# Optimization experiments

Measured on AMD Instinct MI355X. Metric: run time of the kernel, lower is better.

The kernel has to match this reference:

```python
import jax, jax.numpy as jnp
import numpy as np

N = 50000      # nodes
IN = 256       # in_feat
H = 4          # num_heads
DH = 64        # out_feat // num_heads
R = 6          # number of relations
E = 300000     # edges per relation
NEG_SLOPE = 0.2  # DGL GATConv leaky_relu slope


def setup_inputs() -> dict:
    key = jax.random.key(0)
    ks = jax.random.split(key, 7)
    x = jax.random.normal(ks[0], (N, IN), dtype=jnp.float32)
    W = jax.random.normal(ks[1], (R, IN, H * DH), dtype=jnp.float32) * (1.0 / np.sqrt(IN))
    attn_l = jax.random.normal(ks[2], (R, H, DH), dtype=jnp.float32) * 0.1
    attn_r = jax.random.normal(ks[3], (R, H, DH), dtype=jnp.float32) * 0.1
    bias = jax.random.normal(ks[4], (R, H * DH), dtype=jnp.float32) * 0.01
    src = jax.random.randint(ks[5], (R, E), 0, N, dtype=jnp.int32).astype(jnp.int64)
    dst = jax.random.randint(ks[6], (R, E), 0, N, dtype=jnp.int32).astype(jnp.int64)
    return {"x": x, "W": W, "attn_l": attn_l, "attn_r": attn_r, "bias": bias,
            "src": src, "dst": dst}


def reference(x, W, attn_l, attn_r, bias, src, dst):
    n = x.shape[0]
    r_total, h, dh = attn_l.shape
    out = jnp.zeros((n, h, dh), dtype=x.dtype)
    # small fixed loop over structurally-distinct relations (HeteroGraphConv)
    for r in range(r_total):
        feat = (x @ W[r]).reshape(n, h, dh)            # [N,H,Dh] shared src/dst proj
        el = jnp.sum(feat * attn_l[r], axis=-1)        # [N,H]
        er = jnp.sum(feat * attn_r[r], axis=-1)        # [N,H]
        s, d = src[r], dst[r]
        e = jax.nn.leaky_relu(el[s] + er[d], NEG_SLOPE)  # [E,H]
        # segmented softmax over incoming edges of each dst node
        m = jax.ops.segment_max(e, d, num_segments=n)    # [N,H]
        m = jnp.where(jnp.isfinite(m), m, 0.0)
        a = jnp.exp(e - m[d])                            # [E,H]
        z = jax.ops.segment_sum(a, d, num_segments=n)    # [N,H]
        alpha = a / jnp.maximum(z[d], 1e-9)              # [E,H]
        msg = alpha[:, :, None] * feat[s]                # [E,H,Dh]
        agg = jax.ops.segment_sum(msg, d, num_segments=n)  # [N,H,Dh]
        # GATConv: bias + activation(relu) per relation, HeteroGraphConv sums
        out = out + jax.nn.relu(agg + bias[r].reshape(h, dh))
    hcat = out.reshape(n, h * dh)                        # merge='cat' view
    return jax.nn.relu(hcat)                             # layer-level activation
```

## Files before the change

### kernel.cpp

```cpp
#include <hip/hip_runtime.h>

#define NN 50000
#define MP 50048
#define NH 4
#define NR 6
#define NE 300000
#define HD 256
#define SLOTS 32
#define CHUNKS 64
#define CHSZ ((NE + CHUNKS - 1) / CHUNKS)

typedef __attribute__((ext_vector_type(4))) float f32x4;
typedef __attribute__((ext_vector_type(8))) short bf16x8;

__device__ __forceinline__ short f2bf(float f) {
  unsigned u = __float_as_uint(f);
  unsigned r = (u + 0x7FFFu + ((u >> 16) & 1u)) >> 16;
  return (short)r;
}
__device__ __forceinline__ float bf2f_lo(unsigned d) {
  return __uint_as_float(d << 16);
}
__device__ __forceinline__ float bf2f_hi(unsigned d) {
  return __uint_as_float(d & 0xffff0000u);
}

#define GLOAD_LDS16(g, l)                                                     \
  __builtin_amdgcn_global_load_lds(                                           \
      (const __attribute__((address_space(1))) void*)(g),                     \
      (__attribute__((address_space(3))) void*)(l), 16, 0, 0)

__global__ __launch_bounds__(256) void cast_x_kernel(
    const float* __restrict__ x, short* __restrict__ xb, int n4) {
  const int i = blockIdx.x * 256 + threadIdx.x;
  if (i >= n4) return;
  const float4 v = ((const float4*)x)[i];
  short4 o;
  o.x = f2bf(v.x); o.y = f2bf(v.y); o.z = f2bf(v.z); o.w = f2bf(v.w);
  ((short4*)xb)[i] = o;
}

__global__ __launch_bounds__(256) void cast_wt_kernel(
    const float* __restrict__ W, short* __restrict__ wt) {
  const int o = blockIdx.x * 256 + threadIdx.x;
  if (o >= NR * 256 * 256) return;
  const int r = o >> 16;
  const int nrow = (o >> 8) & 255;
  const int k = o & 255;
  wt[o] = f2bf(W[r * 65536 + k * 256 + nrow]);
}

__global__ __launch_bounds__(256) void gemm_kernel(
    const short* __restrict__ xb,
    const short* __restrict__ wt_all,
    const float* __restrict__ attn_l,
    const float* __restrict__ attn_r,
    short* __restrict__ featb_all,
    float* __restrict__ el_all, float* __restrict__ er_all) {
  __shared__ short As[128 * 32];
  __shared__ short Bs[128 * 32];
  const int t = threadIdx.x;
  const int lane = t & 63;
  const int w = t >> 6;
  const int wm = w & 1, wn = w >> 1;
  const int row0 = blockIdx.x * 128;
  const int n0 = blockIdx.y * 128;
  const int r = blockIdx.z;
  const short* wt = wt_all + (size_t)r * 65536;
  short* featb = featb_all + (size_t)r * MP * 256;

  f32x4 acc[4][4];
#pragma unroll
  for (int mi = 0; mi < 4; ++mi)
#pragma unroll
    for (int ni = 0; ni < 4; ++ni) {
      f32x4 z = {0.f, 0.f, 0.f, 0.f};
      acc[mi][ni] = z;
    }

  const int c0 = t, c1 = 256 + t;
  int ar0 = row0 + (c0 >> 2); if (ar0 >= NN) ar0 = NN - 1;
  int ar1 = row0 + (c1 >> 2); if (ar1 >= NN) ar1 = NN - 1;
  const short* ag0 = xb + (size_t)ar0 * 256 + (c0 & 3) * 8;
  const short* ag1 = xb + (size_t)ar1 * 256 + (c1 & 3) * 8;
  const short* bg0 = wt + (size_t)(n0 + (c0 >> 2)) * 256 + (c0 & 3) * 8;
  const short* bg1 = wt + (size_t)(n0 + (c1 >> 2)) * 256 + (c1 & 3) * 8;
  short* la0 = As + c0 * 8;
  short* la1 = As + c1 * 8;
  short* lb0 = Bs + c0 * 8;
  short* lb1 = Bs + c1 * 8;

  const int ra = lane & 15;
  const int qa = (lane >> 4) * 8;

  for (int k0 = 0; k0 < 256; k0 += 32) {
    GLOAD_LDS16(ag0 + k0, la0);
    GLOAD_LDS16(ag1 + k0, la1);
    GLOAD_LDS16(bg0 + k0, lb0);
    GLOAD_LDS16(bg1 + k0, lb1);
    __syncthreads();
    bf16x8 af[4], bfr[4];
#pragma unroll
    for (int mi = 0; mi < 4; ++mi)
      af[mi] = *(const bf16x8*)&As[(wm * 64 + mi * 16 + ra) * 32 + qa];
#pragma unroll
    for (int ni = 0; ni < 4; ++ni)
      bfr[ni] = *(const bf16x8*)&Bs[(wn * 64 + ni * 16 + ra) * 32 + qa];
#pragma unroll
    for (int mi = 0; mi < 4; ++mi)
#pragma unroll
      for (int ni = 0; ni < 4; ++ni)
        acc[mi][ni] = __builtin_amdgcn_mfma_f32_16x16x32_bf16(
            af[mi], bfr[ni], acc[mi][ni], 0, 0, 0);
    __syncthreads();
  }

  const int h = (n0 >> 6) + wn;
  float alv[4], arv[4];
#pragma unroll
  for (int ni = 0; ni < 4; ++ni) {
    alv[ni] = attn_l[r * HD + h * 64 + ni * 16 + ra];
    arv[ni] = attn_r[r * HD + h * 64 + ni * 16 + ra];
  }
#pragma unroll
  for (int mi = 0; mi < 4; ++mi) {
#pragma unroll
    for (int j = 0; j < 4; ++j) {
      const int row = row0 + wm * 64 + mi * 16 + (lane >> 4) * 4 + j;
      float elp = 0.f, erp = 0.f;
#pragma unroll
      for (int ni = 0; ni < 4; ++ni) {
        const float v = acc[mi][ni][j];
        featb[(size_t)row * 256 + n0 + wn * 64 + ni * 16 + ra] = f2bf(v);
        elp = fmaf(v, alv[ni], elp);
        erp = fmaf(v, arv[ni], erp);
      }
#pragma unroll
      for (int m = 1; m < 16; m <<= 1) {
        elp += __shfl_xor(elp, m, 64);
        erp += __shfl_xor(erp, m, 64);
      }
      if (ra == 0 && row < NN) {
        el_all[((size_t)r * NN + row) * NH + h] = elp;
        er_all[((size_t)r * NN + row) * NH + h] = erp;
      }
    }
  }
}

__global__ __launch_bounds__(256) void pack_kernel(
    const int* __restrict__ src, const int* __restrict__ dst,
    unsigned* __restrict__ pe) {
  const int i = blockIdx.x * 256 + threadIdx.x;
  if (i < NR * NE)
    pe[i] = ((unsigned)dst[i] << 16) | (unsigned)src[i];
}

__global__ __launch_bounds__(256) void build_kernel(
    const unsigned* __restrict__ pe, int* __restrict__ deg,
    unsigned short* __restrict__ slots) {
  const int grp = blockIdx.x & 7;
  const int chunk = blockIdx.x >> 3;
  const int lo = chunk * CHSZ;
  const int hi = (lo + CHSZ < NE) ? lo + CHSZ : NE;
  const unsigned dlo = grp * (NN / 8);
  for (int r = 0; r < NR; ++r) {
    for (int i = lo + threadIdx.x; i < hi; i += 256) {
      const unsigned p = pe[(size_t)r * NE + i];
      const unsigned d = p >> 16;
      if (d - dlo < (unsigned)(NN / 8)) {
        const int g = r * NN + (int)d;
        const int sl = atomicAdd(&deg[g], 1);
        if (sl < SLOTS)
          slots[(size_t)g * SLOTS + sl] = (unsigned short)(p & 0xffffu);
      }
    }
  }
}

__global__ __launch_bounds__(256) void agg_kernel(
    const short* __restrict__ featb_all, const float* __restrict__ el_all,
    const float* __restrict__ er_all, const int* __restrict__ deg,
    const unsigned short* __restrict__ slots, const float* __restrict__ bias,
    float* __restrict__ out) {
  const int wid = (blockIdx.x * 256 + threadIdx.x) >> 6;
  const int lane = threadIdx.x & 63;
  if (wid >= NN) return;
  const int half = lane >> 5;
  const int cl = lane & 31;
  const int h = cl >> 3;
  const int c0 = cl * 8;

  float oacc[8];
#pragma unroll
  for (int k = 0; k < 8; ++k) oacc[k] = 0.f;

  for (int r = 0; r < NR; ++r) {
    const int g = r * NN + wid;
    int dg = deg[g];
    dg = dg > SLOTS ? SLOTS : dg;
    const unsigned short* slp = slots + (size_t)g * SLOTS;
    const int sv = (lane < SLOTS) ? (int)slp[lane] : 0;
    const float er_nh = er_all[(size_t)g * NH + h];
    const float* elr = el_all + (size_t)r * NN * NH;
    const short* fb = featb_all + (size_t)r * MP * 256;

    float z = 0.f;
    float acc[8];
#pragma unroll
    for (int k = 0; k < 8; ++k) acc[k] = 0.f;

    const int iters = (dg + 1) >> 1;
    for (int j = 0; j < iters; ++j) {
      const int j2 = 2 * j + half;
      const bool valid = j2 < dg;
      int s = __shfl(sv, j2, 64);
      s = valid ? s : 0;
      float e = elr[s * NH + h] + er_nh;
      e = fmaxf(e, 0.2f * e);
      const float p = valid ? __expf(e) : 0.f;
      const uint4 raw = *(const uint4*)(fb + (size_t)s * 256 + c0);
      z += p;
      acc[0] = fmaf(p, bf2f_lo(raw.x), acc[0]);
      acc[1] = fmaf(p, bf2f_hi(raw.x), acc[1]);
      acc[2] = fmaf(p, bf2f_lo(raw.y), acc[2]);
      acc[3] = fmaf(p, bf2f_hi(raw.y), acc[3]);
      acc[4] = fmaf(p, bf2f_lo(raw.z), acc[4]);
      acc[5] = fmaf(p, bf2f_hi(raw.z), acc[5]);
      acc[6] = fmaf(p, bf2f_lo(raw.w), acc[6]);
      acc[7] = fmaf(p, bf2f_hi(raw.w), acc[7]);
    }
    z += __shfl_xor(z, 32, 64);
#pragma unroll
    for (int k = 0; k < 8; ++k) acc[k] += __shfl_xor(acc[k], 32, 64);
    const float inv = 1.f / fmaxf(z, 1e-9f);
    const float4 b0 = *(const float4*)(bias + r * HD + c0);
    const float4 b1 = *(const float4*)(bias + r * HD + c0 + 4);
    oacc[0] += fmaxf(fmaf(acc[0], inv, b0.x), 0.f);
    oacc[1] += fmaxf(fmaf(acc[1], inv, b0.y), 0.f);
    oacc[2] += fmaxf(fmaf(acc[2], inv, b0.z), 0.f);
    oacc[3] += fmaxf(fmaf(acc[3], inv, b0.w), 0.f);
    oacc[4] += fmaxf(fmaf(acc[4], inv, b1.x), 0.f);
    oacc[5] += fmaxf(fmaf(acc[5], inv, b1.y), 0.f);
    oacc[6] += fmaxf(fmaf(acc[6], inv, b1.z), 0.f);
    oacc[7] += fmaxf(fmaf(acc[7], inv, b1.w), 0.f);
  }
  if (half == 0) {
    float4 s0 = {oacc[0], oacc[1], oacc[2], oacc[3]};
    float4 s1 = {oacc[4], oacc[5], oacc[6], oacc[7]};
    *(float4*)(out + (size_t)wid * 256 + c0) = s0;
    *(float4*)(out + (size_t)wid * 256 + c0 + 4) = s1;
  }
}

extern "C" void kernel_launch(void* const* d_in, const int* in_sizes, int n_in,
                              void* d_out, int out_size, void* d_ws,
                              size_t ws_size, hipStream_t stream) {
  const float* x      = (const float*)d_in[0];
  const float* W      = (const float*)d_in[1];
  const float* attn_l = (const float*)d_in[2];
  const float* attn_r = (const float*)d_in[3];
  const float* bias   = (const float*)d_in[4];
  const int*   src    = (const int*)d_in[5];
  const int*   dst    = (const int*)d_in[6];
  float* out = (float*)d_out;

  char* p = (char*)d_ws;
  auto alloc = [&](size_t bytes) {
    char* r = p;
    p += (bytes + 255) & ~(size_t)255;
    return r;
  };
  short* xb    = (short*)alloc((size_t)NN * HD * 2);
  short* wt    = (short*)alloc((size_t)NR * 256 * 256 * 2);
  short* featb = (short*)alloc((size_t)NR * MP * 256 * 2);
  float* el    = (float*)alloc((size_t)NR * NN * NH * 4);
  float* er    = (float*)alloc((size_t)NR * NN * NH * 4);
  int*   deg   = (int*)alloc((size_t)NR * NN * 4);
  unsigned short* slots =
      (unsigned short*)alloc((size_t)NR * NN * SLOTS * 2);
  unsigned* pe = (unsigned*)alloc((size_t)NR * NE * 4);

  hipMemsetAsync(deg, 0, (size_t)NR * NN * 4, stream);

  cast_x_kernel<<<(NN * HD / 4 + 255) / 256, 256, 0, stream>>>(x, xb,
                                                               NN * HD / 4);
  cast_wt_kernel<<<(NR * 256 * 256 + 255) / 256, 256, 0, stream>>>(W, wt);
  pack_kernel<<<(NR * NE + 255) / 256, 256, 0, stream>>>(src, dst, pe);
  build_kernel<<<CHUNKS * 8, 256, 0, stream>>>(pe, deg, slots);
  gemm_kernel<<<dim3(MP / 128, 2, NR), 256, 0, stream>>>(xb, wt, attn_l,
                                                         attn_r, featb, el,
                                                         er);
  agg_kernel<<<(NN * 64) / 256, 256, 0, stream>>>(featb, el, er, deg, slots,
                                                  bias, out);
}
```

Measured before the change: 476.5 us.

## Remap aggregation wave to 4 columns per lane with scalarized slot indices

Each 64-lane wave now covers all 256 feature columns, 4 per lane, and processes one neighbor per step across the whole wave. The old scheme split the wave into two halves handling alternate edges and then combined them with cross-lane shuffles. Slot indices are loaded as wide vectors and moved into scalar registers with readfirstlane, replacing the per-edge shuffle. The edge loop is unrolled by 4 so several gathers are in flight at once. This removes the shuffle reduction and the half-idle iteration on odd degrees, at the cost of narrower 8-byte loads per lane, more scalar registers, and each wave walking the full edge list serially.

```diff
diff --git a/kernel.cpp b/kernel.cpp
--- a/kernel.cpp
+++ b/kernel.cpp
@@ -186,71 +186,79 @@
   const int wid = (blockIdx.x * 256 + threadIdx.x) >> 6;
   const int lane = threadIdx.x & 63;
   if (wid >= NN) return;
-  const int half = lane >> 5;
-  const int cl = lane & 31;
-  const int h = cl >> 3;
-  const int c0 = cl * 8;
-
-  float oacc[8];
-#pragma unroll
-  for (int k = 0; k < 8; ++k) oacc[k] = 0.f;
+  const int h = lane >> 4;
+  const int c0 = lane * 4;
+
+  float oacc[4] = {0.f, 0.f, 0.f, 0.f};
+  const int wid_u = __builtin_amdgcn_readfirstlane(wid);
 
   for (int r = 0; r < NR; ++r) {
-    const int g = r * NN + wid;
-    int dg = deg[g];
+    const int g = r * NN + wid_u;
+    int dg = __builtin_amdgcn_readfirstlane(deg[g]);
     dg = dg > SLOTS ? SLOTS : dg;
-    const unsigned short* slp = slots + (size_t)g * SLOTS;
-    const int sv = (lane < SLOTS) ? (int)slp[lane] : 0;
+    const uint4* sp = (const uint4*)(slots + (size_t)g * SLOTS);
+    const uint4 q0 = sp[0], q1 = sp[1], q2 = sp[2], q3 = sp[3];
+    unsigned sdv[16];
+    sdv[0]  = __builtin_amdgcn_readfirstlane(q0.x);
+    sdv[1]  = __builtin_amdgcn_readfirstlane(q0.y);
+    sdv[2]  = __builtin_amdgcn_readfirstlane(q0.z);
+    sdv[3]  = __builtin_amdgcn_readfirstlane(q0.w);
+    sdv[4]  = __builtin_amdgcn_readfirstlane(q1.x);
+    sdv[5]  = __builtin_amdgcn_readfirstlane(q1.y);
+    sdv[6]  = __builtin_amdgcn_readfirstlane(q1.z);
+    sdv[7]  = __builtin_amdgcn_readfirstlane(q1.w);
+    sdv[8]  = __builtin_amdgcn_readfirstlane(q2.x);
+    sdv[9]  = __builtin_amdgcn_readfirstlane(q2.y);
+    sdv[10] = __builtin_amdgcn_readfirstlane(q2.z);
+    sdv[11] = __builtin_amdgcn_readfirstlane(q2.w);
+    sdv[12] = __builtin_amdgcn_readfirstlane(q3.x);
+    sdv[13] = __builtin_amdgcn_readfirstlane(q3.y);
+    sdv[14] = __builtin_amdgcn_readfirstlane(q3.z);
+    sdv[15] = __builtin_amdgcn_readfirstlane(q3.w);
+
     const float er_nh = er_all[(size_t)g * NH + h];
     const float* elr = el_all + (size_t)r * NN * NH;
     const short* fb = featb_all + (size_t)r * MP * 256;
 
     float z = 0.f;
-    float acc[8];
-#pragma unroll
-    for (int k = 0; k < 8; ++k) acc[k] = 0.f;
-
-    const int iters = (dg + 1) >> 1;
-    for (int j = 0; j < iters; ++j) {
-      const int j2 = 2 * j + half;
-      const bool valid = j2 < dg;
-      int s = __shfl(sv, j2, 64);
-      s = valid ? s : 0;
-      float e = elr[s * NH + h] + er_nh;
-      e = fmaxf(e, 0.2f * e);
-      const float p = valid ? __expf(e) : 0.f;
-      const uint4 raw = *(const uint4*)(fb + (size_t)s * 256 + c0);
-      z += p;
-      acc[0] = fmaf(p, bf2f_lo(raw.x), acc[0]);
-      acc[1] = fmaf(p, bf2f_hi(raw.x), acc[1]);
-      acc[2] = fmaf(p, bf2f_lo(raw.y), acc[2]);
-      acc[3] = fmaf(p, bf2f_hi(raw.y), acc[3]);
-      acc[4] = fmaf(p, bf2f_lo(raw.z), acc[4]);
-      acc[5] = fmaf(p, bf2f_hi(raw.z), acc[5]);
-      acc[6] = fmaf(p, bf2f_lo(raw.w), acc[6]);
-      acc[7] = fmaf(p, bf2f_hi(raw.w), acc[7]);
+    float acc[4] = {0.f, 0.f, 0.f, 0.f};
+
+#pragma unroll
+    for (int j0 = 0; j0 < SLOTS; j0 += 4) {
+      if (j0 >= dg) break;
+      float pv[4];
+      uint2 rw[4];
+#pragma unroll
+      for (int k = 0; k < 4; ++k) {
+        const int e = j0 + k;
+        int s = (int)((e & 1) ? (sdv[e >> 1] >> 16) : (sdv[e >> 1] & 0xffffu));
+        const bool v = e < dg;
+        s = v ? s : 0;
+        rw[k] = *(const uint2*)(fb + (size_t)s * 256 + c0);
+        float ev = elr[s * NH + h] + er_nh;
+        ev = fmaxf(ev, 0.2f * ev);
+        pv[k] = v ? __expf(ev) : 0.f;
+      }
+#pragma unroll
+      for (int k = 0; k < 4; ++k) {
+        z += pv[k];
+        acc[0] = fmaf(pv[k], bf2f_lo(rw[k].x), acc[0]);
+        acc[1] = fmaf(pv[k], bf2f_hi(rw[k].x), acc[1]);
+        acc[2] = fmaf(pv[k], bf2f_lo(rw[k].y), acc[2]);
+        acc[3] = fmaf(pv[k], bf2f_hi(rw[k].y), acc[3]);
+      }
     }
-    z += __shfl_xor(z, 32, 64);
-#pragma unroll
-    for (int k = 0; k < 8; ++k) acc[k] += __shfl_xor(acc[k], 32, 64);
+
     const float inv = 1.f / fmaxf(z, 1e-9f);
-    const float4 b0 = *(const float4*)(bias + r * HD + c0);
-    const float4 b1 = *(const float4*)(bias + r * HD + c0 + 4);
-    oacc[0] += fmaxf(fmaf(acc[0], inv, b0.x), 0.f);
-    oacc[1] += fmaxf(fmaf(acc[1], inv, b0.y), 0.f);
-    oacc[2] += fmaxf(fmaf(acc[2], inv, b0.z), 0.f);
-    oacc[3] += fmaxf(fmaf(acc[3], inv, b0.w), 0.f);
-    oacc[4] += fmaxf(fmaf(acc[4], inv, b1.x), 0.f);
-    oacc[5] += fmaxf(fmaf(acc[5], inv, b1.y), 0.f);
-    oacc[6] += fmaxf(fmaf(acc[6], inv, b1.z), 0.f);
-    oacc[7] += fmaxf(fmaf(acc[7], inv, b1.w), 0.f);
-  }
-  if (half == 0) {
-    float4 s0 = {oacc[0], oacc[1], oacc[2], oacc[3]};
-    float4 s1 = {oacc[4], oacc[5], oacc[6], oacc[7]};
-    *(float4*)(out + (size_t)wid * 256 + c0) = s0;
-    *(float4*)(out + (size_t)wid * 256 + c0 + 4) = s1;
-  }
+    const float4 bv = *(const float4*)(bias + r * HD + c0);
+    oacc[0] += fmaxf(fmaf(acc[0], inv, bv.x), 0.f);
+    oacc[1] += fmaxf(fmaf(acc[1], inv, bv.y), 0.f);
+    oacc[2] += fmaxf(fmaf(acc[2], inv, bv.z), 0.f);
+    oacc[3] += fmaxf(fmaf(acc[3], inv, bv.w), 0.f);
+  }
+
+  float4 o4 = {oacc[0], oacc[1], oacc[2], oacc[3]};
+  *(float4*)(out + (size_t)wid * 256 + c0) = o4;
 }
 
 extern "C" void kernel_launch(void* const* d_in, const int* in_sizes, int n_in,
```

Result: no change. 476.1 us (-0.1%).
